# Performance work log

Measured on AMD Instinct MI355X. Metric: run time of the kernel, lower is better.

Reference implementation:

```python
import jax, jax.numpy as jnp
import numpy as np

N_NODES = 50000
N_EDGES = 800000
WINDOWS = 10
F_IN = 128
H1, H2, H_LSTM, OUT = 8, 16, 8, 4


def graph_conv(feat, src, dst, W, b, n_nodes):
    """DGL GraphConv with norm='both'. feat: (T, N, Din), W: (Din, Dout)."""
    e_ones = jnp.ones((src.shape[0],), dtype=feat.dtype)
    deg_out = jnp.clip(jax.ops.segment_sum(e_ones, src, num_segments=n_nodes), 1.0)
    deg_in = jnp.clip(jax.ops.segment_sum(e_ones, dst, num_segments=n_nodes), 1.0)
    norm_src = deg_out ** -0.5  # (N,)
    norm_dst = deg_in ** -0.5   # (N,)

    din, dout = W.shape
    h = feat * norm_src[None, :, None]
    if din > dout:  # DGL applies W before aggregation to shrink edge traffic
        h = h @ W
    # gather at src, scatter-sum to dst, vmapped over the time/window axis
    agg = jax.vmap(lambda f: jax.ops.segment_sum(f[src], dst, num_segments=n_nodes))(h)
    if din <= dout:
        agg = agg @ W
    return agg * norm_dst[None, :, None] + b


def lstm(x, Wih, Whh, bih, bhh):
    """Single-layer LSTM (torch gate order i,f,g,o). x: (T, N, Din) -> (T, N, H)."""
    H = Whh.shape[1]
    n = x.shape[1]
    xg = x @ Wih.T + (bih + bhh)  # precompute input contributions: (T, N, 4H)

    def step(carry, xt):
        h, c = carry
        gates = xt + h @ Whh.T
        i, f, g, o = jnp.split(gates, 4, axis=-1)
        c = jax.nn.sigmoid(f) * c + jax.nn.sigmoid(i) * jnp.tanh(g)
        h = jax.nn.sigmoid(o) * jnp.tanh(c)
        return (h, c), h

    init = (jnp.zeros((n, H), x.dtype), jnp.zeros((n, H), x.dtype))
    _, hs = jax.lax.scan(step, init, xg)
    return hs


def setup_inputs() -> dict:
    key = jax.random.key(0)
    ks = jax.random.split(key, 12)
    feat = jax.random.normal(ks[0], (WINDOWS, N_NODES, F_IN), dtype=jnp.float32)
    src = jax.random.randint(ks[1], (N_EDGES,), 0, N_NODES, dtype=jnp.int32)
    dst = jax.random.randint(ks[2], (N_EDGES,), 0, N_NODES, dtype=jnp.int32)
    s = 0.1
    W1 = jax.random.normal(ks[3], (F_IN, H1), dtype=jnp.float32) * s
    b1 = jnp.zeros((H1,), jnp.float32)
    W2 = jax.random.normal(ks[4], (H1, H2), dtype=jnp.float32) * s
    b2 = jnp.zeros((H2,), jnp.float32)
    Wih = jax.random.normal(ks[5], (4 * H_LSTM, H2), dtype=jnp.float32) * s
    Whh = jax.random.normal(ks[6], (4 * H_LSTM, H_LSTM), dtype=jnp.float32) * s
    bih = jax.random.normal(ks[7], (4 * H_LSTM,), dtype=jnp.float32) * s
    bhh = jax.random.normal(ks[8], (4 * H_LSTM,), dtype=jnp.float32) * s
    Wo = jax.random.normal(ks[9], (H_LSTM, OUT), dtype=jnp.float32) * s
    bo = jnp.zeros((OUT,), jnp.float32)
    return {"feat": feat, "src": src, "dst": dst, "W1": W1, "b1": b1,
            "W2": W2, "b2": b2, "Wih": Wih, "Whh": Whh, "bih": bih,
            "bhh": bhh, "Wo": Wo, "bo": bo}


def reference(feat, src, dst, W1, b1, W2, b2, Wih, Whh, bih, bhh, Wo, bo):
    h = jax.nn.relu(graph_conv(feat, src, dst, W1, b1, N_NODES))  # (T, N, 8)
    h = jax.nn.relu(graph_conv(h, src, dst, W2, b2, N_NODES))     # (T, N, 16)
    hs = lstm(h, Wih, Whh, bih, bhh)                              # (T, N, 8)
    pooled = jnp.max(hs[-1], axis=0, keepdims=True)               # (1, 8) max over nodes
    return jax.nn.sigmoid(pooled @ Wo + bo)                       # (1, 4)
```

## Files before the change

kernel.cpp:

```cpp
#include <hip/hip_runtime.h>
#include <math.h>

#define NN 50000
#define NE 800000
#define TW 10
#define SNP 50048
#define CAP 80
#define TOTAL_B 2048
#define BUILD_B 512
#define NBLK 2000
#define LB 196

static __device__ __forceinline__ float sigf(float x){ return 1.0f/(1.0f+__expf(-x)); }
static __device__ __forceinline__ float tanhfast(float x){
  float e2 = __expf(2.0f*x);
  return 1.0f - 2.0f/(e2 + 1.0f);
}
static __device__ __forceinline__ unsigned f2bf(float f){
  unsigned u = __float_as_uint(f);
  return (u + 0x7FFFu + ((u>>16)&1u)) >> 16;
}
static __device__ __forceinline__ unsigned pack2(float a, float b){
  return f2bf(a) | (f2bf(b) << 16);
}
static __device__ __forceinline__ float bflo(unsigned u){ return __uint_as_float(u << 16); }
static __device__ __forceinline__ float bfhi(unsigned u){ return __uint_as_float(u & 0xFFFF0000u); }

#define ZERO_U4 37536
__global__ void k_zero(uint4* __restrict__ p){
  int i = blockIdx.x*256 + threadIdx.x;
  uint4 z; z.x = 0u; z.y = 0u; z.z = 0u; z.w = 0u;
  if (i < ZERO_U4) p[i] = z;
}

__global__ __launch_bounds__(256) void k_buildconv(const float* __restrict__ feat,
                                                   const float* __restrict__ W1,
                                                   const int* __restrict__ src,
                                                   const int* __restrict__ dst,
                                                   int* __restrict__ dego,
                                                   int* __restrict__ degi,
                                                   int* __restrict__ csrp,
                                                   uint4* __restrict__ h1){
  int tid = threadIdx.x;
  int bid = blockIdx.x;
  if (bid < BUILD_B){
    int gt = bid*256 + tid;
    for (int e = gt; e < NE; e += BUILD_B*256){
      int d = dst[e];
      int s = src[e];
      int p = atomicAdd(&degi[d], 1);
      if (p < CAP) csrp[d*CAP + p] = s;
      atomicAdd(&dego[s], 1);
    }
  } else {
    int cb = bid - BUILD_B;
    const int CONV_B = TOTAL_B - BUILD_B;
    int lane = tid & 15;
    float4 wa[8], wb[8];
    #pragma unroll
    for (int d = 0; d < 8; ++d){
      wa[d] = ((const float4*)W1)[(lane*8 + d)*2 + 0];
      wb[d] = ((const float4*)W1)[(lane*8 + d)*2 + 1];
    }
    int gid = (cb*256 + tid) >> 4;
    const int ngroups = CONV_B*16;
    for (int r = gid; r < TW*NN; r += ngroups){
      const float4* frow = (const float4*)feat + (long long)r*32 + lane*2;
      float4 f0 = frow[0], f1 = frow[1];
      float fs[8] = {f0.x,f0.y,f0.z,f0.w,f1.x,f1.y,f1.z,f1.w};
      float acc[8] = {0,0,0,0,0,0,0,0};
      #pragma unroll
      for (int d = 0; d < 8; ++d){
        float fv = fs[d];
        acc[0] += fv*wa[d].x; acc[1] += fv*wa[d].y; acc[2] += fv*wa[d].z; acc[3] += fv*wa[d].w;
        acc[4] += fv*wb[d].x; acc[5] += fv*wb[d].y; acc[6] += fv*wb[d].z; acc[7] += fv*wb[d].w;
      }
      int b8 = (lane>>3)&1, b4 = (lane>>2)&1, b2 = (lane>>1)&1;
      float s0 = b8 ? acc[0] : acc[4], s1 = b8 ? acc[1] : acc[5];
      float s2 = b8 ? acc[2] : acc[6], s3 = b8 ? acc[3] : acc[7];
      float k0 = b8 ? acc[4] : acc[0], k1 = b8 ? acc[5] : acc[1];
      float k2 = b8 ? acc[6] : acc[2], k3 = b8 ? acc[7] : acc[3];
      k0 += __shfl_xor(s0, 8); k1 += __shfl_xor(s1, 8);
      k2 += __shfl_xor(s2, 8); k3 += __shfl_xor(s3, 8);
      float t0 = b4 ? k0 : k2, t1 = b4 ? k1 : k3;
      float m0 = b4 ? k2 : k0, m1 = b4 ? k3 : k1;
      m0 += __shfl_xor(t0, 4); m1 += __shfl_xor(t1, 4);
      float u1 = b2 ? m0 : m1;
      float v0 = b2 ? m1 : m0;
      v0 += __shfl_xor(u1, 2);
      v0 += __shfl_xor(v0, 1);
      int t = r / NN;
      int n = r - t*NN;
      unsigned u = f2bf(v0) << (b2*16);
      u |= __shfl_xor(u, 2);
      if ((lane & 3) == 0){
        int kk = b8*2 + b4;
        ((unsigned*)h1)[((long long)n*10 + t)*4 + kk] = u;
      }
    }
  }
}

__global__ void k_norm(const int* __restrict__ dego, const int* __restrict__ degi,
                       float* __restrict__ ns, float* __restrict__ nd,
                       unsigned* __restrict__ maxbuf){
  int i = blockIdx.x*256 + threadIdx.x;
  if (i < NN){
    int a = dego[i]; if (a < 1) a = 1;
    int b = degi[i]; if (b < 1) b = 1;
    ns[i] = rsqrtf((float)a);
    nd[i] = rsqrtf((float)b);
  }
  if (blockIdx.x == 0 && threadIdx.x < 8) maxbuf[threadIdx.x] = 0x3FFFFFFFu;
}

#define ACC8(v) { a0 += bflo(v.x); a1 += bfhi(v.x); a2 += bflo(v.y); a3 += bfhi(v.y); \
                  a4 += bflo(v.z); a5 += bfhi(v.z); a6 += bflo(v.w); a7 += bfhi(v.w); }
#define ACC8S(v, sc) { a0 = fmaf(sc, bflo(v.x), a0); a1 = fmaf(sc, bfhi(v.x), a1); \
                       a2 = fmaf(sc, bflo(v.y), a2); a3 = fmaf(sc, bfhi(v.y), a3); \
                       a4 = fmaf(sc, bflo(v.z), a4); a5 = fmaf(sc, bfhi(v.z), a5); \
                       a6 = fmaf(sc, bflo(v.w), a6); a7 = fmaf(sc, bfhi(v.w), a7); }

__global__ __launch_bounds__(256) void k_agg1(const uint4* __restrict__ h1,
                                              const int* __restrict__ degi,
                                              const int* __restrict__ csrp,
                                              const float* __restrict__ ns,
                                              const float* __restrict__ nd,
                                              const float* __restrict__ b1,
                                              uint4* __restrict__ x2p){
  __shared__ float b1s[8];
  int tid = threadIdx.x;
  if (tid < 8) b1s[tid] = b1[tid];
  __syncthreads();
  if (tid >= 250) return;
  int n = blockIdx.x*25 + tid/10;
  int t = tid - (tid/10)*10;
  float a0=0,a1=0,a2=0,a3=0,a4=0,a5=0,a6=0,a7=0;
  int deg = degi[n]; if (deg > CAP) deg = CAP;
  const int* row = csrp + n*CAP;
  int j = 0;
  for (; j + 4 <= deg; j += 4){
    int s0 = row[j], s1 = row[j+1], s2 = row[j+2], s3 = row[j+3];
    float n0 = ns[s0], n1 = ns[s1], n2 = ns[s2], n3 = ns[s3];
    uint4 v0 = h1[(long long)s0*10 + t];
    uint4 v1 = h1[(long long)s1*10 + t];
    uint4 v2 = h1[(long long)s2*10 + t];
    uint4 v3 = h1[(long long)s3*10 + t];
    ACC8S(v0, n0) ACC8S(v1, n1) ACC8S(v2, n2) ACC8S(v3, n3)
  }
  for (; j < deg; ++j){
    int s = row[j];
    float nsv = ns[s];
    uint4 v = h1[(long long)s*10 + t];
    ACC8S(v, nsv)
  }
  float sc = nd[n];
  float osc = ns[n];
  float o0 = fmaxf(a0*sc + b1s[0], 0.f)*osc;
  float o1 = fmaxf(a1*sc + b1s[1], 0.f)*osc;
  float o2 = fmaxf(a2*sc + b1s[2], 0.f)*osc;
  float o3 = fmaxf(a3*sc + b1s[3], 0.f)*osc;
  float o4 = fmaxf(a4*sc + b1s[4], 0.f)*osc;
  float o5 = fmaxf(a5*sc + b1s[5], 0.f)*osc;
  float o6 = fmaxf(a6*sc + b1s[6], 0.f)*osc;
  float o7 = fmaxf(a7*sc + b1s[7], 0.f)*osc;
  uint4 pk;
  pk.x = pack2(o0,o1); pk.y = pack2(o2,o3); pk.z = pack2(o4,o5); pk.w = pack2(o6,o7);
  x2p[(long long)n*10 + t] = pk;
}

__global__ __launch_bounds__(256) void k_agg2(const uint4* __restrict__ x2p,
                                              const int* __restrict__ degi,
                                              const int* __restrict__ csrp,
                                              const float* __restrict__ nd,
                                              const float* __restrict__ W2,
                                              const float* __restrict__ b2,
                                              const float* __restrict__ Wih,
                                              const float* __restrict__ bih,
                                              const float* __restrict__ bhh,
                                              uint4* __restrict__ xg){
  __shared__ float w2[128];
  __shared__ float4 wih[128];
  __shared__ float bsum[32];
  __shared__ float b2s[16];
  int tid = threadIdx.x;
  if (tid < 128){ w2[tid] = W2[tid]; wih[tid] = ((const float4*)Wih)[tid]; }
  if (tid < 32) bsum[tid] = bih[tid] + bhh[tid];
  if (tid < 16) b2s[tid] = b2[tid];
  __syncthreads();
  if (tid >= 250) return;
  int nl = tid/10;
  int t  = tid - nl*10;
  int n = blockIdx.x*25 + nl;
  float a0=0,a1=0,a2=0,a3=0,a4=0,a5=0,a6=0,a7=0;
  int deg = degi[n]; if (deg > CAP) deg = CAP;
  const int* row = csrp + n*CAP;
  int j = 0;
  for (; j + 4 <= deg; j += 4){
    int s0 = row[j], s1 = row[j+1], s2 = row[j+2], s3 = row[j+3];
    uint4 v0 = x2p[(long long)s0*10 + t];
    uint4 v1 = x2p[(long long)s1*10 + t];
    uint4 v2 = x2p[(long long)s2*10 + t];
    uint4 v3 = x2p[(long long)s3*10 + t];
    ACC8(v0) ACC8(v1) ACC8(v2) ACC8(v3)
  }
  for (; j < deg; ++j){
    int s = row[j];
    uint4 v = x2p[(long long)s*10 + t];
    ACC8(v)
  }
  float sc = nd[n];
  float y[16];
  #pragma unroll
  for (int jj = 0; jj < 16; ++jj){
    float s = a0*w2[0*16+jj] + a1*w2[1*16+jj] + a2*w2[2*16+jj] + a3*w2[3*16+jj]
            + a4*w2[4*16+jj] + a5*w2[5*16+jj] + a6*w2[6*16+jj] + a7*w2[7*16+jj];
    y[jj] = fmaxf(s*sc + b2s[jj], 0.f);
  }
  uint4* outp = xg + ((long long)n*10 + t)*4;
  #pragma unroll
  for (int g8 = 0; g8 < 4; ++g8){
    float gv[8];
    #pragma unroll
    for (int c = 0; c < 8; ++c){
      int g = g8*8 + c;
      float s = bsum[g];
      #pragma unroll
      for (int q = 0; q < 4; ++q){
        float4 wv = wih[g*4 + q];
        s += y[q*4+0]*wv.x + y[q*4+1]*wv.y + y[q*4+2]*wv.z + y[q*4+3]*wv.w;
      }
      gv[c] = s;
    }
    uint4 pk;
    pk.x = pack2(gv[0],gv[1]); pk.y = pack2(gv[2],gv[3]);
    pk.z = pack2(gv[4],gv[5]); pk.w = pack2(gv[6],gv[7]);
    outp[g8] = pk;
  }
}

__global__ __launch_bounds__(256) void k_lstm(const uint4* __restrict__ xg,
                                              const float* __restrict__ Whh,
                                              unsigned* __restrict__ maxbuf,
                                              int* __restrict__ done,
                                              const float* __restrict__ Wo,
                                              const float* __restrict__ bo,
                                              float* __restrict__ out){
  __shared__ float4 whh[64];
  __shared__ unsigned smax[8];
  __shared__ int lastflag;
  int tid = threadIdx.x;
  if (tid < 64) whh[tid] = ((const float4*)Whh)[tid];
  if (tid < 8) smax[tid] = 0u;
  __syncthreads();
  int n = blockIdx.x*256 + tid;
  if (n < NN){
    float h[8] = {0,0,0,0,0,0,0,0};
    float c[8] = {0,0,0,0,0,0,0,0};
    const uint4* xr = xg + (long long)n*40;
    for (int t = 0; t < TW; ++t){
      float g[32];
      #pragma unroll
      for (int q = 0; q < 4; ++q){
        uint4 v = xr[t*4 + q];
        g[q*8+0]=bflo(v.x); g[q*8+1]=bfhi(v.x);
        g[q*8+2]=bflo(v.y); g[q*8+3]=bfhi(v.y);
        g[q*8+4]=bflo(v.z); g[q*8+5]=bfhi(v.z);
        g[q*8+6]=bflo(v.w); g[q*8+7]=bfhi(v.w);
      }
      #pragma unroll
      for (int gi = 0; gi < 32; ++gi){
        float4 wa = whh[gi*2+0], wb = whh[gi*2+1];
        g[gi] += h[0]*wa.x + h[1]*wa.y + h[2]*wa.z + h[3]*wa.w
               + h[4]*wb.x + h[5]*wb.y + h[6]*wb.z + h[7]*wb.w;
      }
      #pragma unroll
      for (int j = 0; j < 8; ++j){
        float ig = sigf(g[j]);
        float fg = sigf(g[8+j]);
        float gg = tanhfast(g[16+j]);
        float og = sigf(g[24+j]);
        c[j] = fg*c[j] + ig*gg;
        h[j] = og*tanhfast(c[j]);
      }
    }
    #pragma unroll
    for (int j = 0; j < 8; ++j){
      unsigned b = __float_as_uint(h[j]);
      unsigned u = (b & 0x80000000u) ? ~b : (b | 0x80000000u);
      atomicMax(&smax[j], u);
    }
  }
  __syncthreads();
  if (tid < 8) atomicMax(&maxbuf[tid], smax[tid]);
  __syncthreads();
  if (tid == 0){
    __threadfence();
    int prev = atomicAdd(done, 1);
    lastflag = (prev == LB - 1);
  }
  __syncthreads();
  if (lastflag && tid == 0){
    float m[8];
    #pragma unroll
    for (int j = 0; j < 8; ++j){
      unsigned u = atomicAdd(&maxbuf[j], 0u);
      unsigned b = (u & 0x80000000u) ? (u ^ 0x80000000u) : ~u;
      m[j] = __uint_as_float(b);
    }
    #pragma unroll
    for (int o = 0; o < 4; ++o){
      float s = bo[o];
      #pragma unroll
      for (int k = 0; k < 8; ++k) s += m[k]*Wo[k*4 + o];
      out[o] = 1.0f/(1.0f + __expf(-s));
    }
  }
}

extern "C" void kernel_launch(void* const* d_in, const int* in_sizes, int n_in,
                              void* d_out, int out_size, void* d_ws, size_t ws_size,
                              hipStream_t stream) {
  const float* feat = (const float*)d_in[0];
  const int*   src  = (const int*)d_in[1];
  const int*   dst  = (const int*)d_in[2];
  const float* W1   = (const float*)d_in[3];
  const float* b1   = (const float*)d_in[4];
  const float* W2   = (const float*)d_in[5];
  const float* b2   = (const float*)d_in[6];
  const float* Wih  = (const float*)d_in[7];
  const float* Whh  = (const float*)d_in[8];
  const float* bih  = (const float*)d_in[9];
  const float* bhh  = (const float*)d_in[10];
  const float* Wo   = (const float*)d_in[11];
  const float* bo   = (const float*)d_in[12];
  float* out = (float*)d_out;

  int*      base      = (int*)d_ws;
  int*      dego      = base;
  int*      degi      = base + SNP;
  int*      spare     = base + 2*SNP;
  int*      done      = spare + 50040;
  float*    ns        = (float*)(base + 3*SNP);
  float*    nd        = ns + SNP;
  unsigned* maxbuf    = (unsigned*)(nd + SNP);
  int*      csrp      = (int*)(maxbuf + 64);
  uint4*    h1        = (uint4*)(csrp + NN*CAP);
  uint4*    x2p       = h1 + 500000;
  uint4*    xg        = x2p + 500000;

  const int B = 256;
  k_zero     <<<(ZERO_U4 + B - 1)/B, B, 0, stream>>>((uint4*)d_ws);
  k_buildconv<<<TOTAL_B, B, 0, stream>>>(feat, W1, src, dst, dego, degi, csrp, h1);
  k_norm     <<<(NN + B - 1)/B, B, 0, stream>>>(dego, degi, ns, nd, maxbuf);
  k_agg1     <<<NBLK, B, 0, stream>>>(h1, degi, csrp, ns, nd, b1, x2p);
  k_agg2     <<<NBLK, B, 0, stream>>>(x2p, degi, csrp, nd, W2, b2, Wih, bih, bhh, xg);
  k_lstm     <<<LB, B, 0, stream>>>(xg, Whh, maxbuf, done, Wo, bo, out);
}
```

Measured before the change: 257.4 us.

## Drop norm kernel, compute degree norms inline, run CSR build in every block

Removes the separate k_norm launch: inverse-sqrt degree norms are computed on the fly from the degree counters inside the aggregation kernels, and the maxbuf init moves into k_zero. The buildconv kernel no longer splits blocks into build and conv roles. Every block first does a vectorized int4 CSR/degree build pass, then the feat@W1 projection. This saves a launch and the norm arrays' write and read. The cost is extra rsqrt work per gathered edge and a serialized atomic phase ahead of the conv work in every block.

```diff
diff --git a/kernel.cpp b/kernel.cpp
--- a/kernel.cpp
+++ b/kernel.cpp
@@ -7,7 +7,6 @@
 #define SNP 50048
 #define CAP 80
 #define TOTAL_B 2048
-#define BUILD_B 512
 #define NBLK 2000
 #define LB 196
 
@@ -25,12 +24,14 @@
 }
 static __device__ __forceinline__ float bflo(unsigned u){ return __uint_as_float(u << 16); }
 static __device__ __forceinline__ float bfhi(unsigned u){ return __uint_as_float(u & 0xFFFF0000u); }
+static __device__ __forceinline__ float rdeg(int d){ return rsqrtf((float)(d < 1 ? 1 : d)); }
 
 #define ZERO_U4 37536
-__global__ void k_zero(uint4* __restrict__ p){
+__global__ void k_zero(uint4* __restrict__ p, unsigned* __restrict__ maxbuf){
   int i = blockIdx.x*256 + threadIdx.x;
   uint4 z; z.x = 0u; z.y = 0u; z.z = 0u; z.w = 0u;
   if (i < ZERO_U4) p[i] = z;
+  if (i < 8) maxbuf[i] = 0x3FFFFFFFu;
 }
 
 __global__ __launch_bounds__(256) void k_buildconv(const float* __restrict__ feat,
@@ -42,76 +43,71 @@
                                                    int* __restrict__ csrp,
                                                    uint4* __restrict__ h1){
   int tid = threadIdx.x;
-  int bid = blockIdx.x;
-  if (bid < BUILD_B){
-    int gt = bid*256 + tid;
-    for (int e = gt; e < NE; e += BUILD_B*256){
-      int d = dst[e];
-      int s = src[e];
-      int p = atomicAdd(&degi[d], 1);
-      if (p < CAP) csrp[d*CAP + p] = s;
-      atomicAdd(&dego[s], 1);
-    }
-  } else {
-    int cb = bid - BUILD_B;
-    const int CONV_B = TOTAL_B - BUILD_B;
-    int lane = tid & 15;
-    float4 wa[8], wb[8];
+  int gthread = blockIdx.x*256 + tid;
+  {
+    const int4* s4 = (const int4*)src;
+    const int4* d4 = (const int4*)dst;
+    const int NITEM = NE/4;
+    for (int i = gthread; i < NITEM; i += TOTAL_B*256){
+      int4 sv = s4[i];
+      int4 dv = d4[i];
+      int p0 = atomicAdd(&degi[dv.x], 1);
+      int p1 = atomicAdd(&degi[dv.y], 1);
+      int p2 = atomicAdd(&degi[dv.z], 1);
+      int p3 = atomicAdd(&degi[dv.w], 1);
+      if (p0 < CAP) csrp[dv.x*CAP + p0] = sv.x;
+      if (p1 < CAP) csrp[dv.y*CAP + p1] = sv.y;
+      if (p2 < CAP) csrp[dv.z*CAP + p2] = sv.z;
+      if (p3 < CAP) csrp[dv.w*CAP + p3] = sv.w;
+      atomicAdd(&dego[sv.x], 1);
+      atomicAdd(&dego[sv.y], 1);
+      atomicAdd(&dego[sv.z], 1);
+      atomicAdd(&dego[sv.w], 1);
+    }
+  }
+  int lane = tid & 15;
+  float4 wa[8], wb[8];
+  #pragma unroll
+  for (int d = 0; d < 8; ++d){
+    wa[d] = ((const float4*)W1)[(lane*8 + d)*2 + 0];
+    wb[d] = ((const float4*)W1)[(lane*8 + d)*2 + 1];
+  }
+  int gid = gthread >> 4;
+  const int ngroups = TOTAL_B*16;
+  for (int r = gid; r < TW*NN; r += ngroups){
+    const float4* frow = (const float4*)feat + (long long)r*32 + lane*2;
+    float4 f0 = frow[0], f1 = frow[1];
+    float fs[8] = {f0.x,f0.y,f0.z,f0.w,f1.x,f1.y,f1.z,f1.w};
+    float acc[8] = {0,0,0,0,0,0,0,0};
     #pragma unroll
     for (int d = 0; d < 8; ++d){
-      wa[d] = ((const float4*)W1)[(lane*8 + d)*2 + 0];
-      wb[d] = ((const float4*)W1)[(lane*8 + d)*2 + 1];
-    }
-    int gid = (cb*256 + tid) >> 4;
-    const int ngroups = CONV_B*16;
-    for (int r = gid; r < TW*NN; r += ngroups){
-      const float4* frow = (const float4*)feat + (long long)r*32 + lane*2;
-      float4 f0 = frow[0], f1 = frow[1];
-      float fs[8] = {f0.x,f0.y,f0.z,f0.w,f1.x,f1.y,f1.z,f1.w};
-      float acc[8] = {0,0,0,0,0,0,0,0};
-      #pragma unroll
-      for (int d = 0; d < 8; ++d){
-        float fv = fs[d];
-        acc[0] += fv*wa[d].x; acc[1] += fv*wa[d].y; acc[2] += fv*wa[d].z; acc[3] += fv*wa[d].w;
-        acc[4] += fv*wb[d].x; acc[5] += fv*wb[d].y; acc[6] += fv*wb[d].z; acc[7] += fv*wb[d].w;
-      }
-      int b8 = (lane>>3)&1, b4 = (lane>>2)&1, b2 = (lane>>1)&1;
-      float s0 = b8 ? acc[0] : acc[4], s1 = b8 ? acc[1] : acc[5];
-      float s2 = b8 ? acc[2] : acc[6], s3 = b8 ? acc[3] : acc[7];
-      float k0 = b8 ? acc[4] : acc[0], k1 = b8 ? acc[5] : acc[1];
-      float k2 = b8 ? acc[6] : acc[2], k3 = b8 ? acc[7] : acc[3];
-      k0 += __shfl_xor(s0, 8); k1 += __shfl_xor(s1, 8);
-      k2 += __shfl_xor(s2, 8); k3 += __shfl_xor(s3, 8);
-      float t0 = b4 ? k0 : k2, t1 = b4 ? k1 : k3;
-      float m0 = b4 ? k2 : k0, m1 = b4 ? k3 : k1;
-      m0 += __shfl_xor(t0, 4); m1 += __shfl_xor(t1, 4);
-      float u1 = b2 ? m0 : m1;
-      float v0 = b2 ? m1 : m0;
-      v0 += __shfl_xor(u1, 2);
-      v0 += __shfl_xor(v0, 1);
-      int t = r / NN;
-      int n = r - t*NN;
-      unsigned u = f2bf(v0) << (b2*16);
-      u |= __shfl_xor(u, 2);
-      if ((lane & 3) == 0){
-        int kk = b8*2 + b4;
-        ((unsigned*)h1)[((long long)n*10 + t)*4 + kk] = u;
-      }
-    }
-  }
-}
-
-__global__ void k_norm(const int* __restrict__ dego, const int* __restrict__ degi,
-                       float* __restrict__ ns, float* __restrict__ nd,
-                       unsigned* __restrict__ maxbuf){
-  int i = blockIdx.x*256 + threadIdx.x;
-  if (i < NN){
-    int a = dego[i]; if (a < 1) a = 1;
-    int b = degi[i]; if (b < 1) b = 1;
-    ns[i] = rsqrtf((float)a);
-    nd[i] = rsqrtf((float)b);
-  }
-  if (blockIdx.x == 0 && threadIdx.x < 8) maxbuf[threadIdx.x] = 0x3FFFFFFFu;
+      float fv = fs[d];
+      acc[0] += fv*wa[d].x; acc[1] += fv*wa[d].y; acc[2] += fv*wa[d].z; acc[3] += fv*wa[d].w;
+      acc[4] += fv*wb[d].x; acc[5] += fv*wb[d].y; acc[6] += fv*wb[d].z; acc[7] += fv*wb[d].w;
+    }
+    int b8 = (lane>>3)&1, b4 = (lane>>2)&1, b2 = (lane>>1)&1;
+    float s0 = b8 ? acc[0] : acc[4], s1 = b8 ? acc[1] : acc[5];
+    float s2 = b8 ? acc[2] : acc[6], s3 = b8 ? acc[3] : acc[7];
+    float k0 = b8 ? acc[4] : acc[0], k1 = b8 ? acc[5] : acc[1];
+    float k2 = b8 ? acc[6] : acc[2], k3 = b8 ? acc[7] : acc[3];
+    k0 += __shfl_xor(s0, 8); k1 += __shfl_xor(s1, 8);
+    k2 += __shfl_xor(s2, 8); k3 += __shfl_xor(s3, 8);
+    float t0 = b4 ? k0 : k2, t1 = b4 ? k1 : k3;
+    float m0 = b4 ? k2 : k0, m1 = b4 ? k3 : k1;
+    m0 += __shfl_xor(t0, 4); m1 += __shfl_xor(t1, 4);
+    float u1 = b2 ? m0 : m1;
+    float v0 = b2 ? m1 : m0;
+    v0 += __shfl_xor(u1, 2);
+    v0 += __shfl_xor(v0, 1);
+    int t = r / NN;
+    int n = r - t*NN;
+    unsigned u = f2bf(v0) << (b2*16);
+    u |= __shfl_xor(u, 2);
+    if ((lane & 3) == 0){
+      int kk = b8*2 + b4;
+      ((unsigned*)h1)[((long long)n*10 + t)*4 + kk] = u;
+    }
+  }
 }
 
 #define ACC8(v) { a0 += bflo(v.x); a1 += bfhi(v.x); a2 += bflo(v.y); a3 += bfhi(v.y); \
@@ -122,10 +118,9 @@
                        a6 = fmaf(sc, bflo(v.w), a6); a7 = fmaf(sc, bfhi(v.w), a7); }
 
 __global__ __launch_bounds__(256) void k_agg1(const uint4* __restrict__ h1,
+                                              const int* __restrict__ dego,
                                               const int* __restrict__ degi,
                                               const int* __restrict__ csrp,
-                                              const float* __restrict__ ns,
-                                              const float* __restrict__ nd,
                                               const float* __restrict__ b1,
                                               uint4* __restrict__ x2p){
   __shared__ float b1s[8];
@@ -141,7 +136,8 @@
   int j = 0;
   for (; j + 4 <= deg; j += 4){
     int s0 = row[j], s1 = row[j+1], s2 = row[j+2], s3 = row[j+3];
-    float n0 = ns[s0], n1 = ns[s1], n2 = ns[s2], n3 = ns[s3];
+    float n0 = rdeg(dego[s0]), n1 = rdeg(dego[s1]);
+    float n2 = rdeg(dego[s2]), n3 = rdeg(dego[s3]);
     uint4 v0 = h1[(long long)s0*10 + t];
     uint4 v1 = h1[(long long)s1*10 + t];
     uint4 v2 = h1[(long long)s2*10 + t];
@@ -150,12 +146,12 @@
   }
   for (; j < deg; ++j){
     int s = row[j];
-    float nsv = ns[s];
+    float nsv = rdeg(dego[s]);
     uint4 v = h1[(long long)s*10 + t];
     ACC8S(v, nsv)
   }
-  float sc = nd[n];
-  float osc = ns[n];
+  float sc  = rdeg(degi[n]);
+  float osc = rdeg(dego[n]);
   float o0 = fmaxf(a0*sc + b1s[0], 0.f)*osc;
   float o1 = fmaxf(a1*sc + b1s[1], 0.f)*osc;
   float o2 = fmaxf(a2*sc + b1s[2], 0.f)*osc;
@@ -172,7 +168,6 @@
 __global__ __launch_bounds__(256) void k_agg2(const uint4* __restrict__ x2p,
                                               const int* __restrict__ degi,
                                               const int* __restrict__ csrp,
-                                              const float* __restrict__ nd,
                                               const float* __restrict__ W2,
                                               const float* __restrict__ b2,
                                               const float* __restrict__ Wih,
@@ -209,7 +204,7 @@
     uint4 v = x2p[(long long)s*10 + t];
     ACC8(v)
   }
-  float sc = nd[n];
+  float sc = rdeg(degi[n]);
   float y[16];
   #pragma unroll
   for (int jj = 0; jj < 16; ++jj){
@@ -341,19 +336,16 @@
   int*      degi      = base + SNP;
   int*      spare     = base + 2*SNP;
   int*      done      = spare + 50040;
-  float*    ns        = (float*)(base + 3*SNP);
-  float*    nd        = ns + SNP;
-  unsigned* maxbuf    = (unsigned*)(nd + SNP);
+  unsigned* maxbuf    = (unsigned*)(base + 3*SNP);
   int*      csrp      = (int*)(maxbuf + 64);
   uint4*    h1        = (uint4*)(csrp + NN*CAP);
   uint4*    x2p       = h1 + 500000;
   uint4*    xg        = x2p + 500000;
 
   const int B = 256;
-  k_zero     <<<(ZERO_U4 + B - 1)/B, B, 0, stream>>>((uint4*)d_ws);
+  k_zero     <<<(ZERO_U4 + B - 1)/B, B, 0, stream>>>((uint4*)d_ws, maxbuf);
   k_buildconv<<<TOTAL_B, B, 0, stream>>>(feat, W1, src, dst, dego, degi, csrp, h1);
-  k_norm     <<<(NN + B - 1)/B, B, 0, stream>>>(dego, degi, ns, nd, maxbuf);
-  k_agg1     <<<NBLK, B, 0, stream>>>(h1, degi, csrp, ns, nd, b1, x2p);
-  k_agg2     <<<NBLK, B, 0, stream>>>(x2p, degi, csrp, nd, W2, b2, Wih, bih, bhh, xg);
+  k_agg1     <<<NBLK, B, 0, stream>>>(h1, dego, degi, csrp, b1, x2p);
+  k_agg2     <<<NBLK, B, 0, stream>>>(x2p, degi, csrp, W2, b2, Wih, bih, bhh, xg);
   k_lstm     <<<LB, B, 0, stream>>>(xg, Whh, maxbuf, done, Wo, bo, out);
 }
```

Result: no change. 254.4 us (-1.2%).
